# Kernel optimization log

Measured on AMD Instinct MI355X. Metric: run time of the kernel, lower is better.

The kernel has to match this reference:

```python
import jax, jax.numpy as jnp
import numpy as np

NU = NI = 100_000  # nodes per ntype
E = 500_000        # edges per metapath graph
M = 2              # metapaths per ntype
D = 64             # in_size == out_size (num_heads = 1)
H = 128            # semantic-attention hidden
B = 8192           # batch of (user, pos, neg) indices
LRELU = 0.2        # DGL GATConv leaky-relu slope
EPS = 1e-5


def setup_inputs() -> dict:
    key = jax.random.key(0)
    ks = iter(jax.random.split(key, 40))
    rn = lambda sh, s=0.1: jax.random.normal(next(ks), sh, jnp.float32) * s
    ri = lambda sh, hi: jax.random.randint(next(ks), sh, 0, hi, jnp.int32)
    return dict(
        user_idx=ri((B,), NU), item_idx=ri((B,), NI), neg_item_idx=ri((B,), NI),
        user_feat=rn((NU, D), 1.0), item_feat=rn((NI, D), 1.0),
        u_src=ri((M, E), NU), u_dst=ri((M, E), NU),
        i_src=ri((M, E), NI), i_dst=ri((M, E), NI),
        u_W=rn((M, D, D)), u_al=rn((M, D)), u_ar=rn((M, D)), u_b=rn((M, D)),
        i_W=rn((M, D, D)), i_al=rn((M, D)), i_ar=rn((M, D)), i_b=rn((M, D)),
        u_saW1=rn((D, H)), u_sab1=rn((H,)), u_saW2=rn((H, 1)),
        i_saW1=rn((D, H)), i_sab1=rn((H,)), i_saW2=rn((H, 1)),
        userW=rn((D, D)), userb=rn((D,)), itemW=rn((D, D)), itemb=rn((D,)),
        ln_g=jnp.ones((D,), jnp.float32), ln_b=jnp.zeros((D,), jnp.float32),
    )


def _gat_stack(h, W, al, ar, b, src, dst, n_nodes):
    # One GATConv (single head) per metapath, vmapped over the metapath axis.
    def one(Wm, alm, arm, bm, s, d):
        feat = h @ Wm                               # (N, D)
        el = feat @ alm                             # (N,)
        er = feat @ arm                             # (N,)
        e = jax.nn.leaky_relu(el[s] + er[d], LRELU)  # (E,)
        m = jax.ops.segment_max(e, d, num_segments=n_nodes)
        ex = jnp.exp(e - m[d])
        den = jax.ops.segment_sum(ex, d, num_segments=n_nodes)
        alpha = ex / (den[d] + 1e-9)                # per-dst edge softmax
        out = jax.ops.segment_sum(alpha[:, None] * feat[s], d, num_segments=n_nodes)
        return jax.nn.elu(out + bm)                 # (N, D)
    return jax.vmap(one)(W, al, ar, b, src, dst)    # (M, N, D)


def _semantic_attention(z, W1, b1, W2):
    # z: (M, N, D) -> (N, D)
    w = jnp.mean(jnp.tanh(jnp.einsum('mnd,dh->mnh', z, W1) + b1) @ W2, axis=1)  # (M, 1)
    beta = jax.nn.softmax(w, axis=0)                 # softmax over metapaths
    return jnp.sum(beta[:, :, None] * z, axis=0)     # (N, D) -- beta (M,1)->(M,1,1)


def _layernorm(x, g, b):
    mu = x.mean(-1, keepdims=True)
    v = ((x - mu) ** 2).mean(-1, keepdims=True)
    return g * (x - mu) / jnp.sqrt(v + EPS) + b


def reference(user_idx, item_idx, neg_item_idx, user_feat, item_feat,
              u_src, u_dst, i_src, i_dst,
              u_W, u_al, u_ar, u_b, i_W, i_al, i_ar, i_b,
              u_saW1, u_sab1, u_saW2, i_saW1, i_sab1, i_saW2,
              userW, userb, itemW, itemb, ln_g, ln_b):
    zu = _gat_stack(user_feat, u_W, u_al, u_ar, u_b, u_src, u_dst, NU)
    zi = _gat_stack(item_feat, i_W, i_al, i_ar, i_b, i_src, i_dst, NI)
    user_emb = _semantic_attention(zu, u_saW1, u_sab1, u_saW2)
    item_emb = _semantic_attention(zi, i_saW1, i_sab1, i_saW2)
    user_emb = _layernorm(jax.nn.relu(user_emb @ userW + userb), ln_g, ln_b)
    item_emb = _layernorm(jax.nn.relu(item_emb @ itemW + itemb), ln_g, ln_b)
    return (user_emb[user_idx], item_emb[item_idx], item_emb[neg_item_idx])
```

## Files before the change

kernel.cpp:

```cpp
#include <hip/hip_runtime.h>
#include <math.h>

#define N_NODES 100000
#define N_EDGES 500000
#define BATCH   8192
#define NBLK    98
#define HISTX   512
#define FEATX   256

typedef __bf16 bf16;
typedef __bf16 bf16x8 __attribute__((ext_vector_type(8)));
typedef float  f32x4  __attribute__((ext_vector_type(4)));
typedef unsigned long long u64;

#define MFMA16(a, b, c) __builtin_amdgcn_mfma_f32_16x16x32_bf16((a), (b), (c), 0, 0, 0)

__device__ __forceinline__ float wave_reduce_sum(float v) {
    #pragma unroll
    for (int off = 32; off; off >>= 1) v += __shfl_xor(v, off);
    return v;
}

__device__ __forceinline__ float fast_tanh(float x) {
    float e = __expf(2.f * x);
    return 1.f - 2.f / (e + 1.f);
}

__device__ __forceinline__ float b2f(unsigned short u) {
    return __int_as_float(((int)u) << 16);
}

__global__ void __launch_bounds__(256, 6)
fh_all(const float* __restrict__ uf, const float* __restrict__ itf,
       const float* __restrict__ uW, const float* __restrict__ iW,
       const float* __restrict__ ual, const float* __restrict__ ial,
       const float* __restrict__ uar, const float* __restrict__ iar,
       bf16* __restrict__ feat, float* __restrict__ el, float* __restrict__ er,
       const int* __restrict__ udst, const int* __restrict__ idst,
       int* __restrict__ cnt, int* __restrict__ rank, int E, int N) {
    __shared__ bf16x8 ldsW[8][64];
    const int g = blockIdx.y;
    if (blockIdx.x < HISTX) {
        const int* dst = ((g < 2) ? udst : idst) + (size_t)(g & 1) * E;
        int* cntg = cnt + (size_t)g * N;
        int* rk = rank + (size_t)g * E;
        const int tid = blockIdx.x * blockDim.x + threadIdx.x;
        const int stride = HISTX * blockDim.x;
        for (int i0 = tid; i0 < E; i0 += 4 * stride) {
            const int i1 = i0 + stride, i2 = i0 + 2 * stride, i3 = i0 + 3 * stride;
            int d0 = dst[i0];
            int d1 = (i1 < E) ? dst[i1] : 0;
            int d2 = (i2 < E) ? dst[i2] : 0;
            int d3 = (i3 < E) ? dst[i3] : 0;
            int r0 = 0, r1 = 0, r2 = 0, r3 = 0;
            r0 = atomicAdd(&cntg[d0], 1);
            if (i1 < E) r1 = atomicAdd(&cntg[d1], 1);
            if (i2 < E) r2 = atomicAdd(&cntg[d2], 1);
            if (i3 < E) r3 = atomicAdd(&cntg[d3], 1);
            rk[i0] = r0;
            if (i1 < E) rk[i1] = r1;
            if (i2 < E) rk[i2] = r2;
            if (i3 < E) rk[i3] = r3;
        }
        return;
    }
    const int t = g >> 1, m = g & 1;
    const int fx = (int)blockIdx.x - HISTX;
    const float* h   = t ? itf : uf;
    const float* Wm  = (t ? iW : uW) + (size_t)m * 4096;
    const float* alb = (t ? ial : ual) + m * 64;
    const float* arb = (t ? iar : uar) + m * 64;
    for (int f = threadIdx.x; f < 8 * 64; f += blockDim.x) {
        int id = f >> 6, l = f & 63;
        int lc = l & 15, lq = l >> 4;
        int nt = id >> 1, kf = id & 1;
        bf16x8 v;
        #pragma unroll
        for (int j = 0; j < 8; ++j)
            v[j] = (bf16)Wm[(kf * 32 + lq * 8 + j) * 64 + nt * 16 + lc];
        ldsW[id][l] = v;
    }
    __syncthreads();
    const int lane = threadIdx.x & 63, wave = threadIdx.x >> 6, wpb = blockDim.x >> 6;
    const int c = lane & 15, q = lane >> 4;
    float alv[4], arv[4];
    #pragma unroll
    for (int nt = 0; nt < 4; ++nt) {
        alv[nt] = alb[nt * 16 + c];
        arv[nt] = arb[nt * 16 + c];
    }
    const f32x4 zf = {0.f, 0.f, 0.f, 0.f};
    const int tiles = N >> 4;
    bf16* fg   = feat + (size_t)g * N * 64;
    float* elg = el + (size_t)g * N;
    float* erg = er + (size_t)g * N;
    for (int tile = fx * wpb + wave; tile < tiles; tile += FEATX * wpb) {
        const float* hr = h + (size_t)(tile * 16 + c) * 64 + q * 8;
        f32x4 v0 = *(const f32x4*)hr;
        f32x4 v1 = *(const f32x4*)(hr + 4);
        f32x4 v2 = *(const f32x4*)(hr + 32);
        f32x4 v3 = *(const f32x4*)(hr + 36);
        bf16x8 a0, a1;
        #pragma unroll
        for (int j = 0; j < 4; ++j) {
            a0[j] = (bf16)v0[j]; a0[j + 4] = (bf16)v1[j];
            a1[j] = (bf16)v2[j]; a1[j + 4] = (bf16)v3[j];
        }
        f32x4 acc[4];
        #pragma unroll
        for (int nt = 0; nt < 4; ++nt) {
            acc[nt] = zf;
            acc[nt] = MFMA16(a0, ldsW[nt * 2][lane], acc[nt]);
            acc[nt] = MFMA16(a1, ldsW[nt * 2 + 1][lane], acc[nt]);
        }
        #pragma unroll
        for (int nt = 0; nt < 4; ++nt)
            #pragma unroll
            for (int r = 0; r < 4; ++r)
                fg[(size_t)(tile * 16 + q * 4 + r) * 64 + nt * 16 + c] = (bf16)acc[nt][r];
        #pragma unroll
        for (int r = 0; r < 4; ++r) {
            float se = 0.f, sr = 0.f;
            #pragma unroll
            for (int nt = 0; nt < 4; ++nt) {
                se = fmaf(acc[nt][r], alv[nt], se);
                sr = fmaf(acc[nt][r], arv[nt], sr);
            }
            #pragma unroll
            for (int off = 1; off < 16; off <<= 1) {
                se += __shfl_xor(se, off);
                sr += __shfl_xor(sr, off);
            }
            if (c == 0) {
                elg[tile * 16 + q * 4 + r] = se;
                erg[tile * 16 + q * 4 + r] = sr;
            }
        }
    }
}

__global__ void __launch_bounds__(1024)
scan_fused(const int* __restrict__ cnt, int* __restrict__ offsets,
           u64* __restrict__ status, float* __restrict__ wsum, int N) {
    const int g = blockIdx.y, b = blockIdx.x;
    u64* stg = status + g * 128;
    __shared__ int sh[1024];
    __shared__ int total_s, excl_s;
    const int tid = (int)threadIdx.x;
    const int i = b * 1024 + tid;
    int v = (i < N) ? cnt[(size_t)g * N + i] : 0;
    sh[tid] = v;
    __syncthreads();
    for (int off = 1; off < 1024; off <<= 1) {
        int tv = (tid >= off) ? sh[tid - off] : 0;
        __syncthreads();
        sh[tid] += tv;
        __syncthreads();
    }
    int incl = sh[tid];
    if (tid == 1023) total_s = incl;
    __syncthreads();
    const int total = total_s;
    if (tid == 0) {
        if (b == 0) {
            atomicExch(&stg[0], ((u64)total << 2) | 2ull);
            excl_s = 0;
        } else {
            atomicExch(&stg[b], ((u64)total << 2) | 1ull);
            int excl = 0, pb = b - 1;
            while (true) {
                u64 w = atomicAdd(&stg[pb], 0ull);
                int st = (int)(w & 3ull);
                if (st == 0) { __builtin_amdgcn_s_sleep(1); continue; }
                excl += (int)(w >> 2);
                if (st == 2) break;
                --pb;
            }
            atomicExch(&stg[b], ((u64)(excl + total) << 2) | 2ull);
            excl_s = excl;
        }
        if (b == 0 && g == 0) { wsum[0] = 0.f; wsum[1] = 0.f; wsum[2] = 0.f; wsum[3] = 0.f; }
    }
    __syncthreads();
    const int excl = excl_s;
    if (i < N) offsets[(size_t)g * (N + 1) + i] = excl + incl - v;
    if (b == NBLK - 1 && tid == 1023) offsets[(size_t)g * (N + 1) + N] = excl + incl;
}

__global__ void scatter_all(const int* __restrict__ usrc, const int* __restrict__ udst,
                            const int* __restrict__ isrc, const int* __restrict__ idst,
                            const float* __restrict__ el, const float* __restrict__ er,
                            const int* __restrict__ offsets, const int* __restrict__ rank,
                            int2* __restrict__ epack, int E, int N) {
    const int g = blockIdx.y;
    const int* src = ((g < 2) ? usrc : isrc) + (size_t)(g & 1) * E;
    const int* dst = ((g < 2) ? udst : idst) + (size_t)(g & 1) * E;
    const float* elg = el + (size_t)g * N;
    const float* erg = er + (size_t)g * N;
    const int* offg = offsets + (size_t)g * (N + 1);
    const int* rk = rank + (size_t)g * E;
    int2* ep = epack + (size_t)g * E;
    const int tid = blockIdx.x * blockDim.x + threadIdx.x;
    const int stride = gridDim.x * blockDim.x;
    for (int i0 = tid; i0 < E; i0 += 4 * stride) {
        #pragma unroll
        for (int u = 0; u < 4; ++u) {
            const int i = i0 + u * stride;
            if (i < E) {
                int s = src[i], d = dst[i];
                int pos = offg[d] + rk[i];
                float e = elg[s] + erg[d];
                e = (e >= 0.f) ? e : 0.2f * e;
                ep[pos] = make_int2(s << 7, __float_as_int(__expf(e)));
            }
        }
    }
}

__global__ void agg_all(const unsigned short* __restrict__ feat,
                        const float* __restrict__ ub, const float* __restrict__ ib,
                        const int* __restrict__ offsets, const int2* __restrict__ epack,
                        bf16* __restrict__ z, int E, int N) {
    const int g = blockIdx.y;
    const char* featg = (const char*)(feat + (size_t)g * N * 64);
    const float* bv = ((g < 2) ? ub : ib) + (g & 1) * 64;
    const int* offg = offsets + (size_t)g * (N + 1);
    const int2* ep = epack + (size_t)g * E;
    bf16* zg = z + (size_t)g * N * 64;
    const int lane = threadIdx.x & 63, wave = threadIdx.x >> 6, wpb = blockDim.x >> 6;
    const int lane2 = lane * 2;
    const float bl = bv[lane];
    for (int node0 = blockIdx.x * wpb + wave; node0 < N; node0 += gridDim.x * wpb) {
        const int node = __builtin_amdgcn_readfirstlane(node0);
        const int beg = __builtin_amdgcn_readfirstlane(offg[node]);
        const int end = __builtin_amdgcn_readfirstlane(offg[node + 1]);
        float l = 0.f, acc0 = 0.f, acc1 = 0.f;
        int i = beg;
        for (; i + 4 <= end; i += 4) {
            int2 p0 = ep[i], p1 = ep[i + 1], p2 = ep[i + 2], p3 = ep[i + 3];
            float f0 = b2f(*(const unsigned short*)(featg + (p0.x + lane2)));
            float f1 = b2f(*(const unsigned short*)(featg + (p1.x + lane2)));
            float f2 = b2f(*(const unsigned short*)(featg + (p2.x + lane2)));
            float f3 = b2f(*(const unsigned short*)(featg + (p3.x + lane2)));
            float w0 = __int_as_float(p0.y), w1 = __int_as_float(p1.y);
            float w2 = __int_as_float(p2.y), w3 = __int_as_float(p3.y);
            l += (w0 + w1) + (w2 + w3);
            acc0 = fmaf(w0, f0, acc0);
            acc1 = fmaf(w1, f1, acc1);
            acc0 = fmaf(w2, f2, acc0);
            acc1 = fmaf(w3, f3, acc1);
        }
        for (; i < end; ++i) {
            int2 p = ep[i];
            float w = __int_as_float(p.y);
            l += w;
            acc0 = fmaf(w, b2f(*(const unsigned short*)(featg + (p.x + lane2))), acc0);
        }
        float acc = acc0 + acc1;
        float o = acc / (l + 1e-9f);
        float zz = o + bl;
        zz = (zz > 0.f) ? zz : expm1f(zz);
        zg[(size_t)node * 64 + lane] = (bf16)zz;
    }
}

__global__ void __launch_bounds__(256, 4)
sem_mfma(const bf16* __restrict__ z,
         const float* __restrict__ uW1, const float* __restrict__ iW1,
         const float* __restrict__ ub1, const float* __restrict__ ib1,
         const float* __restrict__ uW2, const float* __restrict__ iW2,
         float* __restrict__ wsum, int N) {
    const int g = blockIdx.y, t = g >> 1;
    const float* W1 = t ? iW1 : uW1;
    const float* b1 = t ? ib1 : ub1;
    const float* W2 = t ? iW2 : uW2;
    __shared__ bf16x8 ldsW[16][64];
    for (int f = threadIdx.x; f < 16 * 64; f += blockDim.x) {
        int id = f >> 6, l = f & 63;
        int lc = l & 15, lq = l >> 4;
        int nt = id >> 1, kf = id & 1;
        bf16x8 v;
        #pragma unroll
        for (int j = 0; j < 8; ++j)
            v[j] = (bf16)W1[(kf * 32 + lq * 8 + j) * 128 + nt * 16 + lc];
        ldsW[id][l] = v;
    }
    __syncthreads();
    const int lane = threadIdx.x & 63, wave = threadIdx.x >> 6, wpb = blockDim.x >> 6;
    const int c = lane & 15, q = lane >> 4;
    float b1v[8], w2v[8];
    #pragma unroll
    for (int nt = 0; nt < 8; ++nt) { b1v[nt] = b1[nt * 16 + c]; w2v[nt] = W2[nt * 16 + c]; }
    const bf16* zg = z + (size_t)g * N * 64;
    const f32x4 zf = {0.f, 0.f, 0.f, 0.f};
    float local = 0.f;
    const int tiles = N >> 4;
    for (int tile = blockIdx.x * wpb + wave; tile < tiles; tile += gridDim.x * wpb) {
        const bf16* zr = zg + (size_t)(tile * 16 + c) * 64;
        bf16x8 a0 = *(const bf16x8*)(zr + q * 8);
        bf16x8 a1 = *(const bf16x8*)(zr + 32 + q * 8);
        f32x4 acc[8];
        #pragma unroll
        for (int nt = 0; nt < 8; ++nt) {
            acc[nt] = zf;
            acc[nt] = MFMA16(a0, ldsW[nt * 2][lane], acc[nt]);
            acc[nt] = MFMA16(a1, ldsW[nt * 2 + 1][lane], acc[nt]);
        }
        #pragma unroll
        for (int nt = 0; nt < 8; ++nt)
            #pragma unroll
            for (int r = 0; r < 4; ++r)
                local += w2v[nt] * fast_tanh(acc[nt][r] + b1v[nt]);
    }
    local = wave_reduce_sum(local);
    if (lane == 0) atomicAdd(&wsum[g], local);
}

__global__ void out_all(const int* __restrict__ uidx, const int* __restrict__ iidx,
                        const int* __restrict__ nidx, const bf16* __restrict__ z,
                        const float* __restrict__ wsum,
                        const float* __restrict__ userW, const float* __restrict__ userb,
                        const float* __restrict__ itemW, const float* __restrict__ itemb,
                        const float* __restrict__ ln_g, const float* __restrict__ ln_b,
                        float* __restrict__ out, int N, int B) {
    const int grp = blockIdx.y;
    const int t = (grp == 0) ? 0 : 1;
    const float* Wt = t ? itemW : userW;
    const float* bt = t ? itemb : userb;
    const int* idx = (grp == 0) ? uidx : ((grp == 1) ? iidx : nidx);
    const bf16* zg = z + (size_t)(t * 2) * N * 64;
    const int lane = threadIdx.x & 63, wave = threadIdx.x >> 6, wpb = blockDim.x >> 6;
    float Wc[64];
    #pragma unroll
    for (int k = 0; k < 64; ++k) Wc[k] = Wt[k * 64 + lane];
    const float btl = bt[lane], gl = ln_g[lane], lbl = ln_b[lane];
    const float invN = 1.f / (float)N;
    float w0 = wsum[t * 2] * invN, w1 = wsum[t * 2 + 1] * invN;
    float mx = fmaxf(w0, w1);
    float e0 = __expf(w0 - mx), e1 = __expf(w1 - mx);
    float bsum = e0 + e1;
    float beta0 = e0 / bsum, beta1 = e1 / bsum;
    for (int r = blockIdx.x * wpb + wave; r < B; r += gridDim.x * wpb) {
        const int urr = __builtin_amdgcn_readfirstlane(r);
        const int un = __builtin_amdgcn_readfirstlane(idx[urr]);
        float e = beta0 * (float)zg[(size_t)un * 64 + lane]
                + beta1 * (float)zg[(size_t)(N + un) * 64 + lane];
        float y = btl;
        #pragma unroll
        for (int k = 0; k < 64; ++k) y = fmaf(__shfl(e, k), Wc[k], y);
        y = fmaxf(y, 0.f);
        float mu = wave_reduce_sum(y) * (1.f / 64.f);
        float d = y - mu;
        float var = wave_reduce_sum(d * d) * (1.f / 64.f);
        out[(size_t)(grp * B + r) * 64 + lane] = gl * d / sqrtf(var + 1e-5f) + lbl;
    }
}

extern "C" void kernel_launch(void* const* d_in, const int* in_sizes, int n_in,
                              void* d_out, int out_size, void* d_ws, size_t ws_size,
                              hipStream_t stream) {
    const int* user_idx = (const int*)d_in[0];
    const int* item_idx = (const int*)d_in[1];
    const int* neg_idx  = (const int*)d_in[2];
    const float* user_feat = (const float*)d_in[3];
    const float* item_feat = (const float*)d_in[4];
    const int* u_src = (const int*)d_in[5];
    const int* u_dst = (const int*)d_in[6];
    const int* i_src = (const int*)d_in[7];
    const int* i_dst = (const int*)d_in[8];
    const float* u_W  = (const float*)d_in[9];
    const float* u_al = (const float*)d_in[10];
    const float* u_ar = (const float*)d_in[11];
    const float* u_b  = (const float*)d_in[12];
    const float* i_W  = (const float*)d_in[13];
    const float* i_al = (const float*)d_in[14];
    const float* i_ar = (const float*)d_in[15];
    const float* i_b  = (const float*)d_in[16];
    const float* u_saW1 = (const float*)d_in[17];
    const float* u_sab1 = (const float*)d_in[18];
    const float* u_saW2 = (const float*)d_in[19];
    const float* i_saW1 = (const float*)d_in[20];
    const float* i_sab1 = (const float*)d_in[21];
    const float* i_saW2 = (const float*)d_in[22];
    const float* userW = (const float*)d_in[23];
    const float* userb = (const float*)d_in[24];
    const float* itemW = (const float*)d_in[25];
    const float* itemb = (const float*)d_in[26];
    const float* ln_g  = (const float*)d_in[27];
    const float* ln_b  = (const float*)d_in[28];

    const int N = N_NODES, E = N_EDGES, B = BATCH;

    char* ws = (char*)d_ws;
    size_t off = 0;
    auto alloc = [&](size_t bytes) -> char* {
        char* p = ws + off;
        off += (bytes + 255) & ~(size_t)255;
        return p;
    };
    bf16* feat   = (bf16*)alloc((size_t)4 * N * 64 * 2);
    bf16* z      = (bf16*)alloc((size_t)4 * N * 64 * 2);
    float* el    = (float*)alloc((size_t)4 * N * 4);
    float* er    = (float*)alloc((size_t)4 * N * 4);
    int* offsets = (int*)alloc((size_t)4 * (N + 1) * 4);
    int* cnt     = (int*)alloc((size_t)4 * N * 4);
    u64* status  = (u64*)alloc((size_t)4 * 128 * 8);
    int* rank    = (int*)alloc((size_t)4 * E * 4);
    int2* epack  = (int2*)alloc((size_t)4 * E * 8);
    float* wsum  = (float*)alloc(16);
    (void)ws_size; (void)in_sizes; (void)n_in; (void)out_size;

    dim3 blk(256);
    hipMemsetAsync(cnt, 0, (size_t)4 * N * 4 + 4096, stream);

    fh_all<<<dim3(HISTX + FEATX, 4), blk, 0, stream>>>(
        user_feat, item_feat, u_W, i_W, u_al, i_al, u_ar, i_ar,
        feat, el, er, u_dst, i_dst, cnt, rank, E, N);
    scan_fused<<<dim3(NBLK, 4), dim3(1024), 0, stream>>>(cnt, offsets, status, wsum, N);
    scatter_all<<<dim3(1024, 4), blk, 0, stream>>>(u_src, u_dst, i_src, i_dst,
                                                   el, er, offsets, rank, epack, E, N);
    agg_all<<<dim3(2048, 4), blk, 0, stream>>>((const unsigned short*)feat, u_b, i_b,
                                               offsets, epack, z, E, N);
    sem_mfma<<<dim3(256, 4), blk, 0, stream>>>(z, u_saW1, i_saW1, u_sab1, i_sab1,
                                               u_saW2, i_saW2, wsum, N);
    out_all<<<dim3(512, 3), blk, 0, stream>>>(user_idx, item_idx, neg_idx, z, wsum,
                                              userW, userb, itemW, itemb, ln_g, ln_b,
                                              (float*)d_out, N, B);
}
```

Before: 338.8 us.

## Privatize destination-degree histogram per XCC to reduce cross-die atomic contention

Counts edges per destination in eight per-XCC copies selected by the hardware XCC id, tagging each edge's rank with its XCC. The scan sums the copies and emits per-XCC sub-offsets, which scatter uses to place edges. This aims to cut cross-die atomic traffic on shared counters, at the cost of a larger memset, eightfold counter reads in the scan and an extra offset table gathered randomly in scatter.

```diff
diff --git a/kernel.cpp b/kernel.cpp
--- a/kernel.cpp
+++ b/kernel.cpp
@@ -28,6 +28,12 @@
 
 __device__ __forceinline__ float b2f(unsigned short u) {
     return __int_as_float(((int)u) << 16);
+}
+
+__device__ __forceinline__ int xcc_id() {
+    int x;
+    asm volatile("s_getreg_b32 %0, hwreg(20, 0, 32)" : "=s"(x));
+    return x & 7;
 }
 
 __global__ void __launch_bounds__(256, 6)
@@ -37,15 +43,17 @@
        const float* __restrict__ uar, const float* __restrict__ iar,
        bf16* __restrict__ feat, float* __restrict__ el, float* __restrict__ er,
        const int* __restrict__ udst, const int* __restrict__ idst,
-       int* __restrict__ cnt, int* __restrict__ rank, int E, int N) {
+       int* __restrict__ cnt8, int* __restrict__ rank, int E, int N) {
     __shared__ bf16x8 ldsW[8][64];
     const int g = blockIdx.y;
     if (blockIdx.x < HISTX) {
+        const int s = xcc_id();
         const int* dst = ((g < 2) ? udst : idst) + (size_t)(g & 1) * E;
-        int* cntg = cnt + (size_t)g * N;
+        int* cntg = cnt8 + ((size_t)s * 4 + g) * N;
         int* rk = rank + (size_t)g * E;
         const int tid = blockIdx.x * blockDim.x + threadIdx.x;
         const int stride = HISTX * blockDim.x;
+        const int stag = s << 24;
         for (int i0 = tid; i0 < E; i0 += 4 * stride) {
             const int i1 = i0 + stride, i2 = i0 + 2 * stride, i3 = i0 + 3 * stride;
             int d0 = dst[i0];
@@ -53,14 +61,14 @@
             int d2 = (i2 < E) ? dst[i2] : 0;
             int d3 = (i3 < E) ? dst[i3] : 0;
             int r0 = 0, r1 = 0, r2 = 0, r3 = 0;
-            r0 = atomicAdd(&cntg[d0], 1);
-            if (i1 < E) r1 = atomicAdd(&cntg[d1], 1);
-            if (i2 < E) r2 = atomicAdd(&cntg[d2], 1);
-            if (i3 < E) r3 = atomicAdd(&cntg[d3], 1);
-            rk[i0] = r0;
-            if (i1 < E) rk[i1] = r1;
-            if (i2 < E) rk[i2] = r2;
-            if (i3 < E) rk[i3] = r3;
+            r0 = __hip_atomic_fetch_add(&cntg[d0], 1, __ATOMIC_RELAXED, __HIP_MEMORY_SCOPE_AGENT);
+            if (i1 < E) r1 = __hip_atomic_fetch_add(&cntg[d1], 1, __ATOMIC_RELAXED, __HIP_MEMORY_SCOPE_AGENT);
+            if (i2 < E) r2 = __hip_atomic_fetch_add(&cntg[d2], 1, __ATOMIC_RELAXED, __HIP_MEMORY_SCOPE_AGENT);
+            if (i3 < E) r3 = __hip_atomic_fetch_add(&cntg[d3], 1, __ATOMIC_RELAXED, __HIP_MEMORY_SCOPE_AGENT);
+            rk[i0] = stag | r0;
+            if (i1 < E) rk[i1] = stag | r1;
+            if (i2 < E) rk[i2] = stag | r2;
+            if (i3 < E) rk[i3] = stag | r3;
         }
         return;
     }
@@ -140,15 +148,27 @@
 }
 
 __global__ void __launch_bounds__(1024)
-scan_fused(const int* __restrict__ cnt, int* __restrict__ offsets,
-           u64* __restrict__ status, float* __restrict__ wsum, int N) {
+scan_fused(const int* __restrict__ cnt8, int* __restrict__ offsets,
+           int* __restrict__ off8, u64* __restrict__ status,
+           float* __restrict__ wsum, int N) {
     const int g = blockIdx.y, b = blockIdx.x;
     u64* stg = status + g * 128;
     __shared__ int sh[1024];
     __shared__ int total_s, excl_s;
     const int tid = (int)threadIdx.x;
     const int i = b * 1024 + tid;
-    int v = (i < N) ? cnt[(size_t)g * N + i] : 0;
+    int c[8];
+    int v = 0;
+    if (i < N) {
+        #pragma unroll
+        for (int s = 0; s < 8; ++s) {
+            c[s] = cnt8[((size_t)s * 4 + g) * N + i];
+            v += c[s];
+        }
+    } else {
+        #pragma unroll
+        for (int s = 0; s < 8; ++s) c[s] = 0;
+    }
     sh[tid] = v;
     __syncthreads();
     for (int off = 1; off < 1024; off <<= 1) {
@@ -183,21 +203,30 @@
     }
     __syncthreads();
     const int excl = excl_s;
-    if (i < N) offsets[(size_t)g * (N + 1) + i] = excl + incl - v;
+    if (i < N) {
+        int base = excl + incl - v;
+        offsets[(size_t)g * (N + 1) + i] = base;
+        int4 o0, o1;
+        int a = base;
+        o0.x = a; a += c[0]; o0.y = a; a += c[1]; o0.z = a; a += c[2]; o0.w = a; a += c[3];
+        o1.x = a; a += c[4]; o1.y = a; a += c[5]; o1.z = a; a += c[6]; o1.w = a;
+        *(int4*)(off8 + ((size_t)g * N + i) * 8)     = o0;
+        *(int4*)(off8 + ((size_t)g * N + i) * 8 + 4) = o1;
+    }
     if (b == NBLK - 1 && tid == 1023) offsets[(size_t)g * (N + 1) + N] = excl + incl;
 }
 
 __global__ void scatter_all(const int* __restrict__ usrc, const int* __restrict__ udst,
                             const int* __restrict__ isrc, const int* __restrict__ idst,
                             const float* __restrict__ el, const float* __restrict__ er,
-                            const int* __restrict__ offsets, const int* __restrict__ rank,
+                            const int* __restrict__ off8, const int* __restrict__ rank,
                             int2* __restrict__ epack, int E, int N) {
     const int g = blockIdx.y;
     const int* src = ((g < 2) ? usrc : isrc) + (size_t)(g & 1) * E;
     const int* dst = ((g < 2) ? udst : idst) + (size_t)(g & 1) * E;
     const float* elg = el + (size_t)g * N;
     const float* erg = er + (size_t)g * N;
-    const int* offg = offsets + (size_t)g * (N + 1);
+    const int* o8 = off8 + (size_t)g * N * 8;
     const int* rk = rank + (size_t)g * E;
     int2* ep = epack + (size_t)g * E;
     const int tid = blockIdx.x * blockDim.x + threadIdx.x;
@@ -208,7 +237,8 @@
             const int i = i0 + u * stride;
             if (i < E) {
                 int s = src[i], d = dst[i];
-                int pos = offg[d] + rk[i];
+                int rv = rk[i];
+                int pos = o8[d * 8 + (rv >> 24)] + (rv & 0xffffff);
                 float e = elg[s] + erg[d];
                 e = (e >= 0.f) ? e : 0.2f * e;
                 ep[pos] = make_int2(s << 7, __float_as_int(__expf(e)));
@@ -403,22 +433,23 @@
     float* el    = (float*)alloc((size_t)4 * N * 4);
     float* er    = (float*)alloc((size_t)4 * N * 4);
     int* offsets = (int*)alloc((size_t)4 * (N + 1) * 4);
-    int* cnt     = (int*)alloc((size_t)4 * N * 4);
+    int* cnt8    = (int*)alloc((size_t)32 * N * 4);
     u64* status  = (u64*)alloc((size_t)4 * 128 * 8);
+    int* off8    = (int*)alloc((size_t)4 * N * 8 * 4);
     int* rank    = (int*)alloc((size_t)4 * E * 4);
     int2* epack  = (int2*)alloc((size_t)4 * E * 8);
     float* wsum  = (float*)alloc(16);
     (void)ws_size; (void)in_sizes; (void)n_in; (void)out_size;
 
     dim3 blk(256);
-    hipMemsetAsync(cnt, 0, (size_t)4 * N * 4 + 4096, stream);
+    hipMemsetAsync(cnt8, 0, (size_t)32 * N * 4 + 4096, stream);
 
     fh_all<<<dim3(HISTX + FEATX, 4), blk, 0, stream>>>(
         user_feat, item_feat, u_W, i_W, u_al, i_al, u_ar, i_ar,
-        feat, el, er, u_dst, i_dst, cnt, rank, E, N);
-    scan_fused<<<dim3(NBLK, 4), dim3(1024), 0, stream>>>(cnt, offsets, status, wsum, N);
+        feat, el, er, u_dst, i_dst, cnt8, rank, E, N);
+    scan_fused<<<dim3(NBLK, 4), dim3(1024), 0, stream>>>(cnt8, offsets, off8, status, wsum, N);
     scatter_all<<<dim3(1024, 4), blk, 0, stream>>>(u_src, u_dst, i_src, i_dst,
-                                                   el, er, offsets, rank, epack, E, N);
+                                                   el, er, off8, rank, epack, E, N);
     agg_all<<<dim3(2048, 4), blk, 0, stream>>>((const unsigned short*)feat, u_b, i_b,
                                                offsets, epack, z, E, N);
     sem_mfma<<<dim3(256, 4), blk, 0, stream>>>(z, u_saW1, i_saW1, u_sab1, i_sab1,
```

Result: slower. 359.1 us (+6.0%).
